# Kernel tuning notes

Measured on AMD Instinct MI355X. Metric: run time of the kernel, lower is better.

Reference implementation:

```python
import jax, jax.numpy as jnp
import numpy as np

K = 20
EPS = 1e-5


def _bn(h, g, b, axes):
    m = jnp.mean(h, axes, keepdims=True)
    v = jnp.var(h, axes, keepdims=True)
    return (h - m) * jax.lax.rsqrt(v + EPS) * g + b


def _edge_feat(h):
    # h: [B,N,D] -> edge features [B,N,K,2D] = concat(central, neighbor-central)
    sq = jnp.sum(h * h, -1)
    # negative squared pairwise distance (larger = closer)
    adj = 2.0 * jnp.einsum('bnd,bmd->bnm', h, h) - sq[:, :, None] - sq[:, None, :]
    idx = jax.lax.top_k(adj, K)[1]  # [B,N,K] nearest (incl. self)
    nbr = jax.vmap(lambda hb, ib: hb[ib])(h, idx)  # [B,N,K,D]
    ctr = jnp.broadcast_to(h[:, :, None, :], nbr.shape)
    return jnp.concatenate([ctr, nbr - ctr], -1)


def _edge_layer(h, W, b, g, be):
    # 1x1 conv over edge features, relu THEN batchnorm (matches torch: bn(relu(conv))), max over K
    ef = _edge_feat(h)
    z = jax.nn.relu(jnp.einsum('bnkc,oc->bnko', ef, W) + b)
    z = _bn(z, g, be, (0, 1, 2))
    return jnp.max(z, axis=2)  # [B,N,O]


def _c1d(h, W, b):
    return jnp.einsum('bcl,oc->bol', h, W) + b[None, :, None]


def _bnc(h, g, b):
    m = jnp.mean(h, (0, 2), keepdims=True)
    v = jnp.var(h, (0, 2), keepdims=True)
    return (h - m) * jax.lax.rsqrt(v + EPS) * g[None, :, None] + b[None, :, None]


def _forward(x, rand_grid, W1, b1, g1, be1, W2, b2, g2, be2, W3, b3, g3, be3,
             W4, b4, g4, be4, W5, b5, g5, be5, lW, lb, lg, lbe,
             dW1, db1, dg1, dbe1, dW2, db2, dg2, dbe2, dW3, db3, dg3, dbe3, dW4, db4):
    pts = jnp.transpose(x, (0, 2, 1))  # [B,N,3]
    x1 = _edge_layer(pts, W1, b1, g1, be1)   # [B,N,64]
    x2 = _edge_layer(x1, W2, b2, g2, be2)    # [B,N,64]
    x3 = _edge_layer(x2, W3, b3, g3, be3)    # [B,N,64]
    x4 = _edge_layer(x3, W4, b4, g4, be4)    # [B,N,128]
    cat = jnp.concatenate([x1, x2, x3, x4], -1)  # [B,N,320]
    z = jax.nn.relu(jnp.einsum('bnc,oc->bno', cat, W5) + b5)
    z = _bn(z, g5, be5, (0, 1))
    glob = jnp.max(z, axis=1)  # [B,1024]
    lat = glob @ lW.T + lb
    lat = jax.nn.relu(_bn(lat, lg, lbe, (0,)))  # [B,1024]
    B, C = lat.shape
    P = rand_grid.shape[2]
    y = jnp.concatenate([rand_grid, jnp.broadcast_to(lat[:, :, None], (B, C, P))], axis=1)  # [B,1026,P]
    h = jax.nn.relu(_bnc(_c1d(y, dW1, db1), dg1, dbe1))
    h = jax.nn.relu(_bnc(_c1d(h, dW2, db2), dg2, dbe2))
    h = jax.nn.relu(_bnc(_c1d(h, dW3, db3), dg3, dbe3))
    return jnp.tanh(_c1d(h, dW4, db4))  # [B,3,P]


def setup_inputs() -> dict:
    key = jax.random.key(0)
    ks = iter(jax.random.split(key, 64))
    B, N, BOT = 8, 2048, 1024
    D = BOT + 2  # 1026
    f32 = jnp.float32

    def w(o, c):
        return jax.random.normal(next(ks), (o, c), dtype=f32) * 0.05

    def bnp(c):
        return jnp.ones((c,), f32), jnp.zeros((c,), f32)

    inp = {
        'x': jax.random.normal(next(ks), (B, 3, N), dtype=f32),
        'rand_grid': jax.random.uniform(next(ks), (B, 2, N), dtype=f32),
    }
    enc = [(64, 6), (64, 128), (64, 128), (128, 128), (1024, 320)]
    for i, (o, c) in enumerate(enc, 1):
        inp[f'W{i}'] = w(o, c)
        inp[f'b{i}'] = jnp.zeros((o,), f32)
        inp[f'g{i}'], inp[f'be{i}'] = bnp(o)
    inp['lW'] = w(BOT, 1024)
    inp['lb'] = jnp.zeros((BOT,), f32)
    inp['lg'], inp['lbe'] = bnp(BOT)
    dec = [(D, D), (D // 2, D), (D // 4, D // 2), (3, D // 4)]
    for i, (o, c) in enumerate(dec, 1):
        inp[f'dW{i}'] = w(o, c)
        inp[f'db{i}'] = jnp.zeros((o,), f32)
        if i < 4:
            inp[f'dg{i}'], inp[f'dbe{i}'] = bnp(o)
    return inp


def reference(x, rand_grid, W1, b1, g1, be1, W2, b2, g2, be2, W3, b3, g3, be3,
              W4, b4, g4, be4, W5, b5, g5, be5, lW, lb, lg, lbe,
              dW1, db1, dg1, dbe1, dW2, db2, dg2, dbe2, dW3, db3, dg3, dbe3, dW4, db4):
    return _forward(x, rand_grid, W1, b1, g1, be1, W2, b2, g2, be2, W3, b3, g3, be3,
                    W4, b4, g4, be4, W5, b5, g5, be5, lW, lb, lg, lbe,
                    dW1, db1, dg1, dbe1, dW2, db2, dg2, dbe2, dW3, db3, dg3, dbe3, dW4, db4)
```

## Files before the change

### kernel.cpp

```cpp
#include <hip/hip_runtime.h>
#include <math.h>

constexpr int NB = 8;
constexpr int NN = 2048;
constexpr int NK = 20;
constexpr int NP = 2048;


__global__ void transpose_x_kernel(const float* __restrict__ x, float* __restrict__ pts) {
  int gid = blockIdx.x * 256 + threadIdx.x;
  if (gid >= NB * NN * 3) return;
  int c = gid % 3;
  int n = (gid / 3) % NN;
  int b = gid / (3 * NN);
  pts[gid] = x[(b * 3 + c) * NN + n];
}

__global__ void transpose_mat_ld(const float* __restrict__ src, float* __restrict__ dst, int R,
                                 int C, int ldd) {
  __shared__ float tile[32][33];
  int c0 = blockIdx.x * 32, r0 = blockIdx.y * 32;
  int tx = threadIdx.x & 31, ty = threadIdx.x >> 5;
  for (int i = ty; i < 32; i += 8) {
    int r = r0 + i, c = c0 + tx;
    tile[i][tx] = (r < R && c < C) ? src[(size_t)r * C + c] : 0.f;
  }
  __syncthreads();
  for (int i = ty; i < 32; i += 8) {
    int c = c0 + i, r = r0 + tx;
    if (r < R && c < C) dst[(size_t)c * ldd + r] = tile[tx][i];
  }
}

template <int D>
__global__ void knn_dist_kernel(const float* __restrict__ h, int ld, int coff, int b0,
                                float* __restrict__ dmat) {
  constexpr int DP = (D == 64) ? 68 : 4;
  __shared__ float sc[64][DP];
  __shared__ float sr[64][DP];
  int t = threadIdx.x;
  int c0 = blockIdx.x * 64;
  int r0 = blockIdx.y * 512;
  int bz = blockIdx.z;
  const float* rows = h + ((size_t)(b0 + bz) * NN) * ld + coff;
  if constexpr (D == 64) {
#pragma unroll
    for (int it = 0; it < 4; it++) {
      int e = t + it * 256;
      int r = e >> 4, q = (e & 15) * 4;
      *(float4*)&sc[r][q] = *(const float4*)&rows[(size_t)(c0 + r) * ld + q];
    }
  } else {
    if (t < 192) {
      int r = t / 3, c = t - r * 3;
      sc[r][c] = rows[(size_t)(c0 + r) * ld + c];
    }
  }
  int tx = t & 15, ty = t >> 4;
  for (int rt = 0; rt < 8; rt++) {
    int rr0 = r0 + rt * 64;
    __syncthreads();
    if constexpr (D == 64) {
#pragma unroll
      for (int it = 0; it < 4; it++) {
        int e = t + it * 256;
        int r = e >> 4, q = (e & 15) * 4;
        *(float4*)&sr[r][q] = *(const float4*)&rows[(size_t)(rr0 + r) * ld + q];
      }
    } else {
      if (t < 192) {
        int r = t / 3, c = t - r * 3;
        sr[r][c] = rows[(size_t)(rr0 + r) * ld + c];
      }
    }
    __syncthreads();
    float acc[4][4] = {};
    if constexpr (D == 64) {
#pragma unroll
      for (int dq = 0; dq < 16; dq++) {
        float4 cc[4], rr[4];
#pragma unroll
        for (int i = 0; i < 4; i++) cc[i] = *(const float4*)&sc[ty + 16 * i][dq * 4];
#pragma unroll
        for (int j = 0; j < 4; j++) rr[j] = *(const float4*)&sr[tx + 16 * j][dq * 4];
#pragma unroll
        for (int i = 0; i < 4; i++)
#pragma unroll
          for (int j = 0; j < 4; j++) {
            float dx = cc[i].x - rr[j].x, dy = cc[i].y - rr[j].y;
            float dz = cc[i].z - rr[j].z, dw = cc[i].w - rr[j].w;
            acc[i][j] = fmaf(dx, dx, acc[i][j]);
            acc[i][j] = fmaf(dy, dy, acc[i][j]);
            acc[i][j] = fmaf(dz, dz, acc[i][j]);
            acc[i][j] = fmaf(dw, dw, acc[i][j]);
          }
      }
    } else {
      float ca[4][3], rb[4][3];
#pragma unroll
      for (int i = 0; i < 4; i++)
#pragma unroll
        for (int d = 0; d < 3; d++) ca[i][d] = sc[ty + 16 * i][d];
#pragma unroll
      for (int j = 0; j < 4; j++)
#pragma unroll
        for (int d = 0; d < 3; d++) rb[j][d] = sr[tx + 16 * j][d];
#pragma unroll
      for (int i = 0; i < 4; i++)
#pragma unroll
        for (int j = 0; j < 4; j++)
#pragma unroll
          for (int d = 0; d < 3; d++) {
            float dd = ca[i][d] - rb[j][d];
            acc[i][j] = fmaf(dd, dd, acc[i][j]);
          }
    }
#pragma unroll
    for (int i = 0; i < 4; i++)
#pragma unroll
      for (int j = 0; j < 4; j++)
        dmat[((size_t)bz * NN + c0 + ty + 16 * i) * NN + rr0 + tx + 16 * j] = -acc[i][j];
  }
}

__global__ void knn_topk_kernel(const float* __restrict__ dmat, int b0, int* __restrict__ idx) {
  int t = threadIdx.x;
  int l = t & 63;
  int w = t >> 6;
  int gr = blockIdx.x * 4 + w;
  int bz = gr >> 11;
  int n = gr & 2047;
  const float* row = dmat + ((size_t)bz * NN + n) * NN;
  float v[32];
#pragma unroll
  for (int j = 0; j < 32; j++) v[j] = row[j * 64 + l];
  int mykm = 0;
  for (int k = 0; k < NK; k++) {
    float bv = v[0];
    int bj = 0;
#pragma unroll
    for (int j = 1; j < 32; j++) {
      if (v[j] > bv) { bv = v[j]; bj = j; }
    }
    int gm = bj * 64 + l;
#pragma unroll
    for (int off = 32; off; off >>= 1) {
      float ov = __shfl_xor(bv, off, 64);
      int om = __shfl_xor(gm, off, 64);
      if (ov > bv || (ov == bv && om < gm)) { bv = ov; gm = om; }
    }
    if (l == k) mykm = gm;
    int jb = gm >> 6, lb = gm & 63;
#pragma unroll
    for (int j = 0; j < 32; j++)
      if (j == jb && l == lb) v[j] = -3e38f;
  }
  if (l < NK) idx[((size_t)((b0 + bz) * NN + n)) * NK + l] = mykm;
}

__global__ void weff_kernel(const float* __restrict__ W, int O, int D, float* __restrict__ Weff) {
  int i = blockIdx.x * 256 + threadIdx.x;
  if (i >= 2 * O * D) return;
  int o = i / D, d = i - o * D;
  float v;
  if (o < O) v = W[(size_t)o * 2 * D + d] - W[(size_t)o * 2 * D + D + d];
  else v = W[(size_t)(o - O) * 2 * D + D + d];
  Weff[i] = v;
}

template <int M2, int D>
__global__ __launch_bounds__(256, 4) void pgemm_kernel(const float* __restrict__ h, int ld,
                                                       int coff, const float* __restrict__ Weff,
                                                       const float* __restrict__ bias,
                                                       float* __restrict__ P) {
  constexpr int O = M2 / 2;
  constexpr int GRP = 256 / M2;
  constexpr int NR = 8 / GRP;
  __shared__ float sh[8][D == 3 ? 4 : 68];
  int t = threadIdx.x;
  int n0 = blockIdx.x * 8;
  const float* base = h + coff;
  if constexpr (D == 64) {
    if (t < 128) {
      int r = t >> 4, q = (t & 15) * 4;
      *(float4*)&sh[r][q] = *(const float4*)&base[(size_t)(n0 + r) * ld + q];
    }
  } else {
    if (t < 24) {
      int r = t / 3, c = t - r * 3;
      sh[r][c] = base[(size_t)(n0 + r) * ld + c];
    }
  }
  __syncthreads();
  int o = t % M2;
  int gi = t / M2;
  float acc[NR];
  float bz = (o < O) ? bias[o] : 0.f;
#pragma unroll
  for (int j = 0; j < NR; j++) acc[j] = bz;
  const float* wr = Weff + (size_t)o * D;
  if constexpr (D == 64) {
#pragma unroll
    for (int d4 = 0; d4 < 16; d4++) {
      float4 w4 = *(const float4*)&wr[d4 * 4];
#pragma unroll
      for (int j = 0; j < NR; j++) {
        float4 e4 = *(const float4*)&sh[gi * NR + j][d4 * 4];
        acc[j] = fmaf(w4.x, e4.x, acc[j]);
        acc[j] = fmaf(w4.y, e4.y, acc[j]);
        acc[j] = fmaf(w4.z, e4.z, acc[j]);
        acc[j] = fmaf(w4.w, e4.w, acc[j]);
      }
    }
  } else {
    float w0 = wr[0], w1 = wr[1], w2 = wr[2];
#pragma unroll
    for (int j = 0; j < NR; j++) {
      int r = gi * NR + j;
      acc[j] = fmaf(w0, sh[r][0], fmaf(w1, sh[r][1], fmaf(w2, sh[r][2], acc[j])));
    }
  }
#pragma unroll
  for (int j = 0; j < NR; j++)
    P[(size_t)(n0 + gi * NR + j) * M2 + o] = acc[j];
}

template <int O>
__global__ __launch_bounds__(256, 8) void combine_kernel(const float* __restrict__ P,
                                                         const int* __restrict__ idx,
                                                         float* __restrict__ zmax,
                                                         float* __restrict__ zmin,
                                                         float* __restrict__ psum,
                                                         float* __restrict__ psq) {
  constexpr int CPB = 256 / O;
  constexpr int M2 = 2 * O;
  __shared__ int sidx[CPB * NK];
  int t = threadIdx.x;
  int bn0 = blockIdx.x * CPB;
  if (t < CPB * NK) sidx[t] = idx[(size_t)bn0 * NK + t];
  __syncthreads();
  int g = t / O, o = t % O;
  int bn = bn0 + g;
  int b = bn >> 11;
  float p1 = P[(size_t)bn * M2 + o];
  const float* P2 = P + (size_t)b * NN * M2 + O + o;
  float s = 0.f, sq = 0.f, mx = -3e38f, mn = 3e38f;
#pragma unroll
  for (int k = 0; k < NK; k++) {
    int nb = sidx[g * NK + k];
    float z = fmaxf(p1 + P2[(size_t)nb * M2], 0.f);
    s += z;
    sq = fmaf(z, z, sq);
    mx = fmaxf(mx, z);
    mn = fminf(mn, z);
  }
  zmax[(size_t)bn * O + o] = mx;
  zmin[(size_t)bn * O + o] = mn;
  psum[(size_t)o * (NB * NN) + bn] = s;
  psq[(size_t)o * (NB * NN) + bn] = sq;
}

__global__ void edge_reduce_kernel(const float* __restrict__ psum, const float* __restrict__ psq,
                                   const float* __restrict__ g, const float* __restrict__ be,
                                   float* __restrict__ scale, float* __restrict__ shift,
                                   double inv_n) {
  int o = blockIdx.x, t = threadIdx.x;
  double s = 0.0, q = 0.0;
  const float* ps = psum + (size_t)o * (NB * NN);
  const float* pq = psq + (size_t)o * (NB * NN);
  for (int i = t; i < NB * NN; i += 256) { s += (double)ps[i]; q += (double)pq[i]; }
  __shared__ double rs[256], rq[256];
  rs[t] = s; rq[t] = q;
  __syncthreads();
  for (int st = 128; st; st >>= 1) {
    if (t < st) { rs[t] += rs[t + st]; rq[t] += rq[t + st]; }
    __syncthreads();
  }
  if (t == 0) {
    double mean = rs[0] * inv_n;
    double var = rq[0] * inv_n - mean * mean;
    double r = 1.0 / sqrt(var + 1e-5);
    double sc = (double)g[o] * r;
    scale[o] = (float)sc;
    shift[o] = (float)((double)be[o] - mean * sc);
  }
}

__global__ void edge_affine_kernel(const float* __restrict__ zmax, const float* __restrict__ zmin,
                                   const float* __restrict__ scale, const float* __restrict__ shift,
                                   float* __restrict__ cat, int O, int coff_out) {
  int gid = blockIdx.x * 256 + threadIdx.x;
  int o = gid % O;
  int bn = gid / O;
  float sc = scale[o];
  float v = (sc >= 0.f) ? zmax[gid] : zmin[gid];
  cat[(size_t)bn * 320 + coff_out + o] = fmaf(sc, v, shift[o]);
}

__global__ __launch_bounds__(256, 2) void gemm5_128_kernel(const float* __restrict__ cat,
                                                           const float* __restrict__ W5t,
                                                           const float* __restrict__ b5,
                                                           float* __restrict__ z5) {
  __shared__ float sA[16][132];
  __shared__ float sB[16][128];
  int t = threadIdx.x;
  int r0 = blockIdx.x * 128, m0 = blockIdx.y * 128;
  int arow = t >> 1, ac = (t & 1) * 8;
  int blr = t >> 4, blc = (t & 15) * 8;
  int tx = t & 15, ty = t >> 4;
  float acc[8][8] = {};
  float rA[8], rB[8];

  auto gload = [&](int c0) {
    const float* pa = &cat[(size_t)(r0 + arow) * 320 + c0 + ac];
    float4 a0 = *(const float4*)pa;
    float4 a1 = *(const float4*)(pa + 4);
    rA[0] = a0.x; rA[1] = a0.y; rA[2] = a0.z; rA[3] = a0.w;
    rA[4] = a1.x; rA[5] = a1.y; rA[6] = a1.z; rA[7] = a1.w;
    const float* pb = &W5t[(size_t)(c0 + blr) * 1024 + m0 + blc];
    float4 b0 = *(const float4*)pb;
    float4 b1 = *(const float4*)(pb + 4);
    rB[0] = b0.x; rB[1] = b0.y; rB[2] = b0.z; rB[3] = b0.w;
    rB[4] = b1.x; rB[5] = b1.y; rB[6] = b1.z; rB[7] = b1.w;
  };
  auto ldswrite = [&]() {
#pragma unroll
    for (int j = 0; j < 8; j++) sA[ac + j][arow] = rA[j];
    float4 w0, w1;
    w0.x = rB[0]; w0.y = rB[1]; w0.z = rB[2]; w0.w = rB[3];
    w1.x = rB[4]; w1.y = rB[5]; w1.z = rB[6]; w1.w = rB[7];
    *(float4*)&sB[blr][blc] = w0;
    *(float4*)&sB[blr][blc + 4] = w1;
  };

  gload(0);
  for (int kt = 0; kt < 20; kt++) {
    __syncthreads();
    ldswrite();
    __syncthreads();
    if (kt + 1 < 20) gload((kt + 1) * 16);
#pragma unroll
    for (int c = 0; c < 16; c++) {
      float4 a0 = *(const float4*)&sA[c][ty * 4];
      float4 a1 = *(const float4*)&sA[c][64 + ty * 4];
      float4 b0 = *(const float4*)&sB[c][tx * 4];
      float4 b1 = *(const float4*)&sB[c][64 + tx * 4];
      float av[8] = {a0.x, a0.y, a0.z, a0.w, a1.x, a1.y, a1.z, a1.w};
      float bv[8] = {b0.x, b0.y, b0.z, b0.w, b1.x, b1.y, b1.z, b1.w};
#pragma unroll
      for (int i = 0; i < 8; i++)
#pragma unroll
        for (int j = 0; j < 8; j++) acc[i][j] = fmaf(av[i], bv[j], acc[i][j]);
    }
  }
  float bj[8];
#pragma unroll
  for (int j = 0; j < 8; j++)
    bj[j] = b5[m0 + (j < 4 ? tx * 4 + j : 64 + tx * 4 + (j - 4))];
#pragma unroll
  for (int i = 0; i < 8; i++) {
    int r = r0 + (i < 4 ? ty * 4 + i : 64 + ty * 4 + (i - 4));
    float* dst = &z5[(size_t)r * 1024 + m0];
    float4 q0, q1;
    q0.x = fmaxf(acc[i][0] + bj[0], 0.f);
    q0.y = fmaxf(acc[i][1] + bj[1], 0.f);
    q0.z = fmaxf(acc[i][2] + bj[2], 0.f);
    q0.w = fmaxf(acc[i][3] + bj[3], 0.f);
    q1.x = fmaxf(acc[i][4] + bj[4], 0.f);
    q1.y = fmaxf(acc[i][5] + bj[5], 0.f);
    q1.z = fmaxf(acc[i][6] + bj[6], 0.f);
    q1.w = fmaxf(acc[i][7] + bj[7], 0.f);
    *(float4*)&dst[tx * 4] = q0;
    *(float4*)&dst[64 + tx * 4] = q1;
  }
}

__global__ void stats5_kernel(const float* __restrict__ z5, double* __restrict__ psum5,
                              double* __restrict__ psq5, float* __restrict__ pmax5,
                              float* __restrict__ pmin5) {
  int j = blockIdx.x, t = threadIdx.x;
  int row0 = j * 64;
  double s0 = 0, s1 = 0, s2 = 0, s3 = 0, q0 = 0, q1 = 0, q2 = 0, q3 = 0;
  float4 mx = {-3e38f, -3e38f, -3e38f, -3e38f}, mn = {3e38f, 3e38f, 3e38f, 3e38f};
  for (int r = 0; r < 64; r++) {
    float4 v = *(const float4*)&z5[(size_t)(row0 + r) * 1024 + t * 4];
    s0 += v.x; s1 += v.y; s2 += v.z; s3 += v.w;
    q0 += (double)v.x * v.x; q1 += (double)v.y * v.y;
    q2 += (double)v.z * v.z; q3 += (double)v.w * v.w;
    mx.x = fmaxf(mx.x, v.x); mx.y = fmaxf(mx.y, v.y); mx.z = fmaxf(mx.z, v.z); mx.w = fmaxf(mx.w, v.w);
    mn.x = fminf(mn.x, v.x); mn.y = fminf(mn.y, v.y); mn.z = fminf(mn.z, v.z); mn.w = fminf(mn.w, v.w);
  }
  size_t base = (size_t)j * 1024 + t * 4;
  psum5[base + 0] = s0; psum5[base + 1] = s1; psum5[base + 2] = s2; psum5[base + 3] = s3;
  psq5[base + 0] = q0; psq5[base + 1] = q1; psq5[base + 2] = q2; psq5[base + 3] = q3;
  *(float4*)&pmax5[base] = mx;
  *(float4*)&pmin5[base] = mn;
}

__global__ void reduce5_glob_kernel(const double* __restrict__ psum5, const double* __restrict__ psq5,
                                    const float* __restrict__ pmax5, const float* __restrict__ pmin5,
                                    const float* __restrict__ g5, const float* __restrict__ be5,
                                    float* __restrict__ glob) {
  int o = blockIdx.x * 256 + threadIdx.x;
  double s = 0.0, q = 0.0;
  for (int j = 0; j < 256; j++) {
    s += psum5[(size_t)j * 1024 + o];
    q += psq5[(size_t)j * 1024 + o];
  }
  double mean = s * (1.0 / 16384.0);
  double var = q * (1.0 / 16384.0) - mean * mean;
  double r = 1.0 / sqrt(var + 1e-5);
  double scd = (double)g5[o] * r;
  float sc = (float)scd;
  float sh = (float)((double)be5[o] - mean * scd);
  for (int b = 0; b < 8; b++) {
    float m;
    if (sc >= 0.f) {
      m = -3e38f;
      for (int jj = 0; jj < 32; jj++) m = fmaxf(m, pmax5[(size_t)(b * 32 + jj) * 1024 + o]);
    } else {
      m = 3e38f;
      for (int jj = 0; jj < 32; jj++) m = fminf(m, pmin5[(size_t)(b * 32 + jj) * 1024 + o]);
    }
    glob[b * 1024 + o] = fmaf(sc, m, sh);
  }
}


__global__ void lat_gemm_kernel(const float* __restrict__ glob, const float* __restrict__ lWt,
                                const float* __restrict__ lb, float* __restrict__ latp) {
  __shared__ float gr[1024];
  int b = blockIdx.x, t = threadIdx.x;
  for (int e = t; e < 1024; e += 256) gr[e] = glob[b * 1024 + e];
  __syncthreads();
  int o = blockIdx.y * 256 + t;
  float acc = lb[o];
  for (int c = 0; c < 1024; c++) acc = fmaf(lWt[(size_t)c * 1024 + o], gr[c], acc);
  latp[b * 1024 + o] = acc;
}

__global__ void lat_bn_kernel(const float* __restrict__ latp, const float* __restrict__ lg,
                              const float* __restrict__ lbe, float* __restrict__ lat) {
  int o = blockIdx.x * 256 + threadIdx.x;
  float v[8];
  double s = 0.0, q = 0.0;
  for (int b = 0; b < 8; b++) {
    v[b] = latp[b * 1024 + o];
    s += (double)v[b];
    q += (double)v[b] * (double)v[b];
  }
  double mean = s * 0.125;
  double var = q * 0.125 - mean * mean;
  double r = 1.0 / sqrt(var + 1e-5);
  double gd = (double)lg[o], bd = (double)lbe[o];
  for (int b = 0; b < 8; b++) {
    float z = (float)(((double)v[b] - mean) * r * gd + bd);
    lat[b * 1024 + o] = fmaxf(z, 0.f);
  }
}

__global__ void dec_u_kernel(const float* __restrict__ lat, const float* __restrict__ dW1t,
                             const float* __restrict__ db1, float* __restrict__ u) {
  __shared__ float ls[1024];
  int b = blockIdx.x, t = threadIdx.x;
  for (int e = t; e < 1024; e += 256) ls[e] = lat[b * 1024 + e];
  __syncthreads();
  int o = blockIdx.y * 256 + t;
  if (o < 1026) {
    float acc = db1[o];
    for (int c = 0; c < 1024; c++) acc = fmaf(dW1t[(size_t)(2 + c) * 1026 + o], ls[c], acc);
    u[b * 1026 + o] = acc;
  }
}

__global__ void dec1_z_kernel(const float* __restrict__ rg, const float* __restrict__ dW1t,
                              const float* __restrict__ u, float* __restrict__ z1) {
  int bo = blockIdx.x;
  int b = bo / 1026;
  int o = bo - b * 1026;
  int t = threadIdx.x;
  float w0 = dW1t[o], w1 = dW1t[1026 + o], ub = u[bo];
  const float4* r0 = (const float4*)(rg + (size_t)b * 2 * NP);
  const float4* r1 = (const float4*)(rg + (size_t)b * 2 * NP + NP);
  float4* zr = (float4*)(z1 + (size_t)bo * NP);
  for (int i = t; i < NP / 4; i += 256) {
    float4 a = r0[i], c = r1[i], rr;
    rr.x = fmaf(w0, a.x, fmaf(w1, c.x, ub));
    rr.y = fmaf(w0, a.y, fmaf(w1, c.y, ub));
    rr.z = fmaf(w0, a.z, fmaf(w1, c.z, ub));
    rr.w = fmaf(w0, a.w, fmaf(w1, c.w, ub));
    zr[i] = rr;
  }
}

__global__ void dstats_kernel(const float* __restrict__ z, int C, const float* __restrict__ g,
                              const float* __restrict__ be, float* __restrict__ scale,
                              float* __restrict__ shift) {
  int o = blockIdx.x, t = threadIdx.x;
  double s = 0.0, q = 0.0;
  for (int b = 0; b < 8; b++) {
    const float4* row = (const float4*)(z + ((size_t)b * C + o) * NP);
    for (int i = t; i < NP / 4; i += 256) {
      float4 v = row[i];
      s += (double)v.x + (double)v.y + (double)v.z + (double)v.w;
      q += (double)v.x * v.x + (double)v.y * v.y + (double)v.z * v.z + (double)v.w * v.w;
    }
  }
  __shared__ double rs[256], rq[256];
  rs[t] = s; rq[t] = q;
  __syncthreads();
  for (int st = 128; st; st >>= 1) {
    if (t < st) { rs[t] += rs[t + st]; rq[t] += rq[t + st]; }
    __syncthreads();
  }
  if (t == 0) {
    double inv = 1.0 / (8.0 * NP);
    double mean = rs[0] * inv;
    double var = rq[0] * inv - mean * mean;
    double r = 1.0 / sqrt(var + 1e-5);
    double sc = (double)g[o] * r;
    scale[o] = (float)sc;
    shift[o] = (float)((double)be[o] - mean * sc);
  }
}

__global__ __launch_bounds__(256, 2) void dec_gemm128_kernel(
    const float* __restrict__ zin, const float* __restrict__ Wt, int ldA,
    const float* __restrict__ bias, const float* __restrict__ scale,
    const float* __restrict__ shift, float* __restrict__ zout, int Ci, int Co) {
  __shared__ float sA[16][128];
  __shared__ float sB[16][128];
  int t = threadIdx.x;
  int m0 = blockIdx.x * 128, p0 = blockIdx.y * 128, b = blockIdx.z;
  int lr = t >> 4, lc = (t & 15) * 8;
  int tx = t & 15, ty = t >> 4;
  int numK = (Ci + 15) >> 4;
  float acc[8][8] = {};
  float rA[8], rB[8];

  auto gload = [&](int kt) {
    int c = kt * 16 + lr;
#pragma unroll
    for (int j = 0; j < 8; j++) { rA[j] = 0.f; rB[j] = 0.f; }
    if (c < Ci) {
      int mb = m0 + lc;
      if (mb + 8 <= Co) {
        float4 a0 = *(const float4*)&Wt[(size_t)c * ldA + mb];
        float4 a1 = *(const float4*)&Wt[(size_t)c * ldA + mb + 4];
        rA[0] = a0.x; rA[1] = a0.y; rA[2] = a0.z; rA[3] = a0.w;
        rA[4] = a1.x; rA[5] = a1.y; rA[6] = a1.z; rA[7] = a1.w;
      } else {
#pragma unroll
        for (int j = 0; j < 8; j++)
          if (mb + j < Co) rA[j] = Wt[(size_t)c * ldA + mb + j];
      }
      float sc = scale[c], sh = shift[c];
      const float* src = &zin[((size_t)b * Ci + c) * NP + p0 + lc];
      float4 z0 = *(const float4*)src;
      float4 z1 = *(const float4*)(src + 4);
      rB[0] = fmaxf(fmaf(sc, z0.x, sh), 0.f);
      rB[1] = fmaxf(fmaf(sc, z0.y, sh), 0.f);
      rB[2] = fmaxf(fmaf(sc, z0.z, sh), 0.f);
      rB[3] = fmaxf(fmaf(sc, z0.w, sh), 0.f);
      rB[4] = fmaxf(fmaf(sc, z1.x, sh), 0.f);
      rB[5] = fmaxf(fmaf(sc, z1.y, sh), 0.f);
      rB[6] = fmaxf(fmaf(sc, z1.z, sh), 0.f);
      rB[7] = fmaxf(fmaf(sc, z1.w, sh), 0.f);
    }
  };
  auto ldswrite = [&]() {
    float4 v0, v1;
    v0.x = rA[0]; v0.y = rA[1]; v0.z = rA[2]; v0.w = rA[3];
    v1.x = rA[4]; v1.y = rA[5]; v1.z = rA[6]; v1.w = rA[7];
    *(float4*)&sA[lr][lc] = v0;
    *(float4*)&sA[lr][lc + 4] = v1;
    v0.x = rB[0]; v0.y = rB[1]; v0.z = rB[2]; v0.w = rB[3];
    v1.x = rB[4]; v1.y = rB[5]; v1.z = rB[6]; v1.w = rB[7];
    *(float4*)&sB[lr][lc] = v0;
    *(float4*)&sB[lr][lc + 4] = v1;
  };

  gload(0);
  for (int kt = 0; kt < numK; kt++) {
    __syncthreads();
    ldswrite();
    __syncthreads();
    if (kt + 1 < numK) gload(kt + 1);
#pragma unroll
    for (int c = 0; c < 16; c++) {
      float4 a0 = *(const float4*)&sA[c][ty * 4];
      float4 a1 = *(const float4*)&sA[c][64 + ty * 4];
      float4 b0 = *(const float4*)&sB[c][tx * 4];
      float4 b1 = *(const float4*)&sB[c][64 + tx * 4];
      float av[8] = {a0.x, a0.y, a0.z, a0.w, a1.x, a1.y, a1.z, a1.w};
      float bv[8] = {b0.x, b0.y, b0.z, b0.w, b1.x, b1.y, b1.z, b1.w};
#pragma unroll
      for (int i = 0; i < 8; i++)
#pragma unroll
        for (int j = 0; j < 8; j++) acc[i][j] = fmaf(av[i], bv[j], acc[i][j]);
    }
  }
#pragma unroll
  for (int i = 0; i < 8; i++) {
    int m = m0 + (i < 4 ? ty * 4 + i : 64 + ty * 4 + (i - 4));
    if (m < Co) {
      float bv = bias[m];
      float* dst = &zout[((size_t)b * Co + m) * NP + p0];
      float4 q0, q1;
      q0.x = acc[i][0] + bv; q0.y = acc[i][1] + bv;
      q0.z = acc[i][2] + bv; q0.w = acc[i][3] + bv;
      q1.x = acc[i][4] + bv; q1.y = acc[i][5] + bv;
      q1.z = acc[i][6] + bv; q1.w = acc[i][7] + bv;
      *(float4*)&dst[tx * 4] = q0;
      *(float4*)&dst[64 + tx * 4] = q1;
    }
  }
}

__global__ void dec_final_kernel(const float* __restrict__ z3, const float* __restrict__ dW4,
                                 const float* __restrict__ db4, const float* __restrict__ scale,
                                 const float* __restrict__ shift, float* __restrict__ out) {
  __shared__ float w4[3 * 256];
  __shared__ float sc[256], sh[256];
  int b = blockIdx.x, pc = blockIdx.y, t = threadIdx.x;
  for (int e = t; e < 768; e += 256) w4[e] = dW4[e];
  sc[t] = scale[t];
  sh[t] = shift[t];
  __syncthreads();
  int p = pc * 256 + t;
  float a0 = 0.f, a1 = 0.f, a2 = 0.f;
  for (int c = 0; c < 256; c++) {
    float hv = fmaxf(fmaf(sc[c], z3[((size_t)(b * 256 + c)) * NP + p], sh[c]), 0.f);
    a0 = fmaf(w4[c], hv, a0);
    a1 = fmaf(w4[256 + c], hv, a1);
    a2 = fmaf(w4[512 + c], hv, a2);
  }
  out[((size_t)b * 3 + 0) * NP + p] = tanhf(a0 + db4[0]);
  out[((size_t)b * 3 + 1) * NP + p] = tanhf(a1 + db4[1]);
  out[((size_t)b * 3 + 2) * NP + p] = tanhf(a2 + db4[2]);
}


extern "C" void kernel_launch(void* const* d_in, const int* in_sizes, int n_in, void* d_out,
                              int out_size, void* d_ws, size_t ws_size, hipStream_t stream) {
  const float* x = (const float*)d_in[0];
  const float* rg = (const float*)d_in[1];
  const float* W1 = (const float*)d_in[2];
  const float* b1 = (const float*)d_in[3];
  const float* g1 = (const float*)d_in[4];
  const float* be1 = (const float*)d_in[5];
  const float* W2 = (const float*)d_in[6];
  const float* b2 = (const float*)d_in[7];
  const float* g2 = (const float*)d_in[8];
  const float* be2 = (const float*)d_in[9];
  const float* W3 = (const float*)d_in[10];
  const float* b3 = (const float*)d_in[11];
  const float* g3 = (const float*)d_in[12];
  const float* be3 = (const float*)d_in[13];
  const float* W4 = (const float*)d_in[14];
  const float* b4 = (const float*)d_in[15];
  const float* g4 = (const float*)d_in[16];
  const float* be4 = (const float*)d_in[17];
  const float* W5 = (const float*)d_in[18];
  const float* b5 = (const float*)d_in[19];
  const float* g5 = (const float*)d_in[20];
  const float* be5 = (const float*)d_in[21];
  const float* lW = (const float*)d_in[22];
  const float* lb = (const float*)d_in[23];
  const float* lg = (const float*)d_in[24];
  const float* lbe = (const float*)d_in[25];
  const float* dW1 = (const float*)d_in[26];
  const float* db1 = (const float*)d_in[27];
  const float* dg1 = (const float*)d_in[28];
  const float* dbe1 = (const float*)d_in[29];
  const float* dW2 = (const float*)d_in[30];
  const float* db2 = (const float*)d_in[31];
  const float* dg2 = (const float*)d_in[32];
  const float* dbe2 = (const float*)d_in[33];
  const float* dW3 = (const float*)d_in[34];
  const float* db3 = (const float*)d_in[35];
  const float* dg3 = (const float*)d_in[36];
  const float* dbe3 = (const float*)d_in[37];
  const float* dW4 = (const float*)d_in[38];
  const float* db4 = (const float*)d_in[39];
  float* out = (float*)d_out;

  float* ws = (float*)d_ws;
  size_t off = 0;
  auto alloc = [&](size_t n) {
    size_t r = off;
    off += (n + 255) & ~(size_t)255;
    return r;
  };
  size_t f_pts = alloc((size_t)NB * NN * 3);
  size_t f_uA = alloc(13959168);
  size_t f_cat = f_uA;
  size_t f_idx = f_cat + 5242880;
  size_t f_zmax = f_idx + 327680;
  size_t f_zmin = f_zmax + 2097152;
  size_t f_psum = f_zmin + 2097152;
  size_t f_psq = f_psum + 2097152;
  size_t f_z2 = f_uA;
  size_t f_uB = alloc(16809984);
  size_t f_z5 = f_uB, f_z1 = f_uB;
  float* dmat = ws + f_uB;
  float* P = ws + f_uB;
  size_t f_uC = alloc(4194304);
  double* ps5_d = (double*)(ws + f_uC);
  double* pq5_d = ps5_d + 262144;
  size_t f_pM5 = f_uC + 2097152;
  size_t f_pm5 = f_pM5 + 262144;
  size_t f_z3 = f_uC;
  size_t f_weff = alloc(256 * 64);
  size_t f_W5t = alloc(320 * 1024);
  size_t f_lWt = alloc(1024 * 1024);
  size_t f_dW1t = alloc((size_t)1026 * 1026);
  size_t f_dW2t = alloc((size_t)1026 * 516);
  size_t f_dW3t = alloc(513 * 256);
  size_t f_scale = alloc(2048);
  size_t f_shift = alloc(2048);
  size_t f_glob = alloc(8 * 1024);
  size_t f_latp = alloc(8 * 1024);
  size_t f_lat = alloc(8 * 1024);
  size_t f_u = alloc(8 * 1026);
  (void)ws_size;
  (void)in_sizes;
  (void)n_in;
  (void)out_size;

  float* cat = ws + f_cat;
  int* idxp = (int*)(ws + f_idx);
  float* zmax = ws + f_zmax;
  float* zmin = ws + f_zmin;
  float* psumf = ws + f_psum;
  float* psqf = ws + f_psq;
  float* weff = ws + f_weff;
  float* scale = ws + f_scale;
  float* shift = ws + f_shift;
  const double invn_e = 1.0 / (double)(NB * NN * NK);

  transpose_x_kernel<<<192, 256, 0, stream>>>(x, ws + f_pts);
  transpose_mat_ld<<<dim3(10, 32), 256, 0, stream>>>(W5, ws + f_W5t, 1024, 320, 1024);
  transpose_mat_ld<<<dim3(32, 32), 256, 0, stream>>>(lW, ws + f_lWt, 1024, 1024, 1024);
  transpose_mat_ld<<<dim3(33, 33), 256, 0, stream>>>(dW1, ws + f_dW1t, 1026, 1026, 1026);
  transpose_mat_ld<<<dim3(33, 17), 256, 0, stream>>>(dW2, ws + f_dW2t, 513, 1026, 516);
  transpose_mat_ld<<<dim3(17, 8), 256, 0, stream>>>(dW3, ws + f_dW3t, 256, 513, 256);

  auto run_knn = [&](const float* h, int ld, int coff, bool d64) {
    for (int bb0 = 0; bb0 < NB; bb0 += 4) {
      if (d64)
        knn_dist_kernel<64><<<dim3(32, 4, 4), 256, 0, stream>>>(h, ld, coff, bb0, dmat);
      else
        knn_dist_kernel<3><<<dim3(32, 4, 4), 256, 0, stream>>>(h, ld, coff, bb0, dmat);
      knn_topk_kernel<<<2048, 256, 0, stream>>>(dmat, bb0, idxp);
    }
  };

  run_knn(ws + f_pts, 3, 0, false);
  weff_kernel<<<2, 256, 0, stream>>>(W1, 64, 3, weff);
  pgemm_kernel<128, 3><<<2048, 256, 0, stream>>>(ws + f_pts, 3, 0, weff, b1, P);
  combine_kernel<64><<<4096, 256, 0, stream>>>(P, idxp, zmax, zmin, psumf, psqf);
  edge_reduce_kernel<<<64, 256, 0, stream>>>(psumf, psqf, g1, be1, scale, shift, invn_e);
  edge_affine_kernel<<<NB * NN * 64 / 256, 256, 0, stream>>>(zmax, zmin, scale, shift, cat, 64, 0);
  run_knn(cat, 320, 0, true);
  weff_kernel<<<32, 256, 0, stream>>>(W2, 64, 64, weff);
  pgemm_kernel<128, 64><<<2048, 256, 0, stream>>>(cat, 320, 0, weff, b2, P);
  combine_kernel<64><<<4096, 256, 0, stream>>>(P, idxp, zmax, zmin, psumf, psqf);
  edge_reduce_kernel<<<64, 256, 0, stream>>>(psumf, psqf, g2, be2, scale, shift, invn_e);
  edge_affine_kernel<<<NB * NN * 64 / 256, 256, 0, stream>>>(zmax, zmin, scale, shift, cat, 64, 64);
  run_knn(cat, 320, 64, true);
  weff_kernel<<<32, 256, 0, stream>>>(W3, 64, 64, weff);
  pgemm_kernel<128, 64><<<2048, 256, 0, stream>>>(cat, 320, 64, weff, b3, P);
  combine_kernel<64><<<4096, 256, 0, stream>>>(P, idxp, zmax, zmin, psumf, psqf);
  edge_reduce_kernel<<<64, 256, 0, stream>>>(psumf, psqf, g3, be3, scale, shift, invn_e);
  edge_affine_kernel<<<NB * NN * 64 / 256, 256, 0, stream>>>(zmax, zmin, scale, shift, cat, 64, 128);
  run_knn(cat, 320, 128, true);
  weff_kernel<<<64, 256, 0, stream>>>(W4, 128, 64, weff);
  pgemm_kernel<256, 64><<<2048, 256, 0, stream>>>(cat, 320, 128, weff, b4, P);
  combine_kernel<128><<<8192, 256, 0, stream>>>(P, idxp, zmax, zmin, psumf, psqf);
  edge_reduce_kernel<<<128, 256, 0, stream>>>(psumf, psqf, g4, be4, scale, shift, invn_e);
  edge_affine_kernel<<<NB * NN * 128 / 256, 256, 0, stream>>>(zmax, zmin, scale, shift, cat, 128, 192);

  gemm5_128_kernel<<<dim3(128, 8), 256, 0, stream>>>(cat, ws + f_W5t, b5, ws + f_z5);
  stats5_kernel<<<256, 256, 0, stream>>>(ws + f_z5, ps5_d, pq5_d, ws + f_pM5, ws + f_pm5);
  reduce5_glob_kernel<<<4, 256, 0, stream>>>(ps5_d, pq5_d, ws + f_pM5, ws + f_pm5, g5, be5,
                                             ws + f_glob);
  lat_gemm_kernel<<<dim3(8, 4), 256, 0, stream>>>(ws + f_glob, ws + f_lWt, lb, ws + f_latp);
  lat_bn_kernel<<<4, 256, 0, stream>>>(ws + f_latp, lg, lbe, ws + f_lat);
  dec_u_kernel<<<dim3(8, 5), 256, 0, stream>>>(ws + f_lat, ws + f_dW1t, db1, ws + f_u);
  dec1_z_kernel<<<8 * 1026, 256, 0, stream>>>(rg, ws + f_dW1t, ws + f_u, ws + f_z1);
  dstats_kernel<<<1026, 256, 0, stream>>>(ws + f_z1, 1026, dg1, dbe1, scale, shift);
  dec_gemm128_kernel<<<dim3(5, 16, 8), 256, 0, stream>>>(ws + f_z1, ws + f_dW2t, 516, db2, scale,
                                                         shift, ws + f_z2, 1026, 513);
  dstats_kernel<<<513, 256, 0, stream>>>(ws + f_z2, 513, dg2, dbe2, scale, shift);
  dec_gemm128_kernel<<<dim3(2, 16, 8), 256, 0, stream>>>(ws + f_z2, ws + f_dW3t, 256, db3, scale,
                                                         shift, ws + f_z3, 513, 256);
  dstats_kernel<<<256, 256, 0, stream>>>(ws + f_z3, 256, dg3, dbe3, scale, shift);
  dec_final_kernel<<<dim3(8, 8), 256, 0, stream>>>(ws + f_z3, dW4, db4, scale, shift, out);
}
```

Before: 1.850 ms.

## Use 128x128 register-tiled kNN distance kernel for 64-dim features

Replaces the D=64 path of the pairwise distance kernel with a new kernel that computes 128x128 output tiles using 8x8 per-thread register blocking. The feature dimension is staged through shared memory in 16-wide transposed chunks, and the next chunk's global load is prefetched while the current one is computed. Outputs are written as float4 vectors. The aim is more arithmetic per shared-memory load and coalesced stores. The cost is a 64-float accumulator per thread, which raises register pressure under launch_bounds(256,2).

After: 1.936 ms. 1.05x slower.

```diff
diff --git a/kernel.cpp b/kernel.cpp
--- a/kernel.cpp
+++ b/kernel.cpp
@@ -35,91 +35,119 @@
 template <int D>
 __global__ void knn_dist_kernel(const float* __restrict__ h, int ld, int coff, int b0,
                                 float* __restrict__ dmat) {
-  constexpr int DP = (D == 64) ? 68 : 4;
-  __shared__ float sc[64][DP];
-  __shared__ float sr[64][DP];
+  __shared__ float sc[64][4];
+  __shared__ float sr[64][4];
   int t = threadIdx.x;
   int c0 = blockIdx.x * 64;
   int r0 = blockIdx.y * 512;
   int bz = blockIdx.z;
   const float* rows = h + ((size_t)(b0 + bz) * NN) * ld + coff;
-  if constexpr (D == 64) {
-#pragma unroll
-    for (int it = 0; it < 4; it++) {
-      int e = t + it * 256;
-      int r = e >> 4, q = (e & 15) * 4;
-      *(float4*)&sc[r][q] = *(const float4*)&rows[(size_t)(c0 + r) * ld + q];
-    }
-  } else {
-    if (t < 192) {
-      int r = t / 3, c = t - r * 3;
-      sc[r][c] = rows[(size_t)(c0 + r) * ld + c];
-    }
+  if (t < 192) {
+    int r = t / 3, c = t - r * 3;
+    sc[r][c] = rows[(size_t)(c0 + r) * ld + c];
   }
   int tx = t & 15, ty = t >> 4;
   for (int rt = 0; rt < 8; rt++) {
     int rr0 = r0 + rt * 64;
     __syncthreads();
-    if constexpr (D == 64) {
-#pragma unroll
-      for (int it = 0; it < 4; it++) {
-        int e = t + it * 256;
-        int r = e >> 4, q = (e & 15) * 4;
-        *(float4*)&sr[r][q] = *(const float4*)&rows[(size_t)(rr0 + r) * ld + q];
-      }
-    } else {
-      if (t < 192) {
-        int r = t / 3, c = t - r * 3;
-        sr[r][c] = rows[(size_t)(rr0 + r) * ld + c];
-      }
+    if (t < 192) {
+      int r = t / 3, c = t - r * 3;
+      sr[r][c] = rows[(size_t)(rr0 + r) * ld + c];
     }
     __syncthreads();
     float acc[4][4] = {};
-    if constexpr (D == 64) {
-#pragma unroll
-      for (int dq = 0; dq < 16; dq++) {
-        float4 cc[4], rr[4];
-#pragma unroll
-        for (int i = 0; i < 4; i++) cc[i] = *(const float4*)&sc[ty + 16 * i][dq * 4];
-#pragma unroll
-        for (int j = 0; j < 4; j++) rr[j] = *(const float4*)&sr[tx + 16 * j][dq * 4];
-#pragma unroll
-        for (int i = 0; i < 4; i++)
-#pragma unroll
-          for (int j = 0; j < 4; j++) {
-            float dx = cc[i].x - rr[j].x, dy = cc[i].y - rr[j].y;
-            float dz = cc[i].z - rr[j].z, dw = cc[i].w - rr[j].w;
-            acc[i][j] = fmaf(dx, dx, acc[i][j]);
-            acc[i][j] = fmaf(dy, dy, acc[i][j]);
-            acc[i][j] = fmaf(dz, dz, acc[i][j]);
-            acc[i][j] = fmaf(dw, dw, acc[i][j]);
-          }
-      }
-    } else {
-      float ca[4][3], rb[4][3];
-#pragma unroll
-      for (int i = 0; i < 4; i++)
-#pragma unroll
-        for (int d = 0; d < 3; d++) ca[i][d] = sc[ty + 16 * i][d];
+    float ca[4][3], rb[4][3];
+#pragma unroll
+    for (int i = 0; i < 4; i++)
+#pragma unroll
+      for (int d = 0; d < 3; d++) ca[i][d] = sc[ty + 16 * i][d];
+#pragma unroll
+    for (int j = 0; j < 4; j++)
+#pragma unroll
+      for (int d = 0; d < 3; d++) rb[j][d] = sr[tx + 16 * j][d];
+#pragma unroll
+    for (int i = 0; i < 4; i++)
 #pragma unroll
       for (int j = 0; j < 4; j++)
 #pragma unroll
-        for (int d = 0; d < 3; d++) rb[j][d] = sr[tx + 16 * j][d];
-#pragma unroll
-      for (int i = 0; i < 4; i++)
-#pragma unroll
-        for (int j = 0; j < 4; j++)
-#pragma unroll
-          for (int d = 0; d < 3; d++) {
-            float dd = ca[i][d] - rb[j][d];
-            acc[i][j] = fmaf(dd, dd, acc[i][j]);
-          }
-    }
+        for (int d = 0; d < 3; d++) {
+          float dd = ca[i][d] - rb[j][d];
+          acc[i][j] = fmaf(dd, dd, acc[i][j]);
+        }
 #pragma unroll
     for (int i = 0; i < 4; i++)
 #pragma unroll
       for (int j = 0; j < 4; j++)
         dmat[((size_t)bz * NN + c0 + ty + 16 * i) * NN + rr0 + tx + 16 * j] = -acc[i][j];
+  }
+}
+
+__global__ __launch_bounds__(256, 2) void knn_dist128_kernel(const float* __restrict__ h, int ld,
+                                                             int coff, int b0,
+                                                             float* __restrict__ dmat) {
+  __shared__ float sc[16][132];
+  __shared__ float sr[16][128];
+  int t = threadIdx.x;
+  int c0 = blockIdx.x * 128, r0 = blockIdx.y * 128;
+  int bz = blockIdx.z;
+  const float* rows = h + ((size_t)(b0 + bz) * NN) * ld + coff;
+  int arow = t >> 1, ac = (t & 1) * 8;
+  int tx = t & 15, ty = t >> 4;
+  float acc[8][8] = {};
+  float rA[8], rB[8];
+
+  auto gload = [&](int d0) {
+    const float* pc = &rows[(size_t)(c0 + arow) * ld + d0 + ac];
+    float4 a0 = *(const float4*)pc;
+    float4 a1 = *(const float4*)(pc + 4);
+    rA[0] = a0.x; rA[1] = a0.y; rA[2] = a0.z; rA[3] = a0.w;
+    rA[4] = a1.x; rA[5] = a1.y; rA[6] = a1.z; rA[7] = a1.w;
+    const float* pr = &rows[(size_t)(r0 + arow) * ld + d0 + ac];
+    float4 b0 = *(const float4*)pr;
+    float4 b1 = *(const float4*)(pr + 4);
+    rB[0] = b0.x; rB[1] = b0.y; rB[2] = b0.z; rB[3] = b0.w;
+    rB[4] = b1.x; rB[5] = b1.y; rB[6] = b1.z; rB[7] = b1.w;
+  };
+  auto ldswrite = [&]() {
+#pragma unroll
+    for (int j = 0; j < 8; j++) {
+      sc[ac + j][arow] = rA[j];
+      sr[ac + j][arow] = rB[j];
+    }
+  };
+
+  gload(0);
+  for (int ks = 0; ks < 4; ks++) {
+    __syncthreads();
+    ldswrite();
+    __syncthreads();
+    if (ks + 1 < 4) gload((ks + 1) * 16);
+#pragma unroll
+    for (int d = 0; d < 16; d++) {
+      float4 a0 = *(const float4*)&sc[d][ty * 4];
+      float4 a1 = *(const float4*)&sc[d][64 + ty * 4];
+      float4 b0 = *(const float4*)&sr[d][tx * 4];
+      float4 b1 = *(const float4*)&sr[d][64 + tx * 4];
+      float av[8] = {a0.x, a0.y, a0.z, a0.w, a1.x, a1.y, a1.z, a1.w};
+      float bv[8] = {b0.x, b0.y, b0.z, b0.w, b1.x, b1.y, b1.z, b1.w};
+#pragma unroll
+      for (int i = 0; i < 8; i++)
+#pragma unroll
+        for (int j = 0; j < 8; j++) {
+          float dd = av[i] - bv[j];
+          acc[i][j] = fmaf(dd, dd, acc[i][j]);
+        }
+    }
+  }
+#pragma unroll
+  for (int i = 0; i < 8; i++) {
+    int c = c0 + (i < 4 ? ty * 4 + i : 64 + ty * 4 + (i - 4));
+    float* dst = &dmat[((size_t)bz * NN + c) * NN + r0];
+    float4 q0, q1;
+    q0.x = -acc[i][0]; q0.y = -acc[i][1]; q0.z = -acc[i][2]; q0.w = -acc[i][3];
+    q1.x = -acc[i][4]; q1.y = -acc[i][5]; q1.z = -acc[i][6]; q1.w = -acc[i][7];
+    *(float4*)&dst[tx * 4] = q0;
+    *(float4*)&dst[64 + tx * 4] = q1;
   }
 }
 
@@ -749,7 +777,7 @@
   auto run_knn = [&](const float* h, int ld, int coff, bool d64) {
     for (int bb0 = 0; bb0 < NB; bb0 += 4) {
       if (d64)
-        knn_dist_kernel<64><<<dim3(32, 4, 4), 256, 0, stream>>>(h, ld, coff, bb0, dmat);
+        knn_dist128_kernel<<<dim3(16, 16, 4), 256, 0, stream>>>(h, ld, coff, bb0, dmat);
       else
         knn_dist_kernel<3><<<dim3(32, 4, 4), 256, 0, stream>>>(h, ld, coff, bb0, dmat);
       knn_topk_kernel<<<2048, 256, 0, stream>>>(dmat, bb0, idxp);
```
